# Optimization experiments

Measured on AMD Instinct MI355X. Metric: run time of the kernel, lower is better.

## Reference

```python
import jax, jax.numpy as jnp
import numpy as np

N_NODES = 100000
N_EDGES = 3200000
NUM_GRAPHS = 128
HIDDEN = 32


def setup_inputs() -> dict:
    key = jax.random.key(0)
    ks = jax.random.split(key, 10)
    x1 = jax.random.normal(ks[0], (N_NODES, 1), dtype=jnp.float32)
    x2 = jax.random.normal(ks[1], (N_NODES, 1), dtype=jnp.float32)
    edge_index1 = jax.random.randint(ks[2], (2, N_EDGES), 0, N_NODES, dtype=jnp.int64)
    edge_index2 = jax.random.randint(ks[3], (2, N_EDGES), 0, N_NODES, dtype=jnp.int64)
    batch1 = jnp.sort(jax.random.randint(ks[4], (N_NODES,), 0, NUM_GRAPHS, dtype=jnp.int64))
    batch2 = jnp.sort(jax.random.randint(ks[5], (N_NODES,), 0, NUM_GRAPHS, dtype=jnp.int64))
    W1 = jax.random.normal(ks[6], (1, HIDDEN), dtype=jnp.float32) * 0.5
    b1 = jax.random.normal(ks[7], (HIDDEN,), dtype=jnp.float32) * 0.1
    W2 = jax.random.normal(ks[8], (HIDDEN, HIDDEN), dtype=jnp.float32) * (1.0 / np.sqrt(HIDDEN))
    b2 = jax.random.normal(ks[9], (HIDDEN,), dtype=jnp.float32) * 0.1
    return {"x1": x1, "edge_index1": edge_index1, "batch1": batch1,
            "x2": x2, "edge_index2": edge_index2, "batch2": batch2,
            "W1": W1, "b1": b1, "W2": W2, "b2": b2}


def _gin_conv(x, src, dst, W, b):
    # GINConv with eps=0: nn(x + sum_{j->i} x_j); messages from src aggregated at dst
    agg = jax.ops.segment_sum(x[src], dst, num_segments=N_NODES)
    return jax.nn.relu((x + agg) @ W + b)  # nn = Linear + ReLU


def _encode(x, edge_index, batch, W1, b1, W2, b2):
    src, dst = edge_index[0], edge_index[1]
    h = _gin_conv(x, src, dst, W1, b1)
    # F.relu after conv1 (idempotent after ReLU inside nn, kept for fidelity)
    h = jax.nn.relu(h)
    h = _gin_conv(h, src, dst, W2, b2)
    # global_add_pool: segment-sum nodes by graph id
    return jax.ops.segment_sum(h, batch, num_segments=NUM_GRAPHS)


def reference(x1, edge_index1, batch1, x2, edge_index2, batch2, W1, b1, W2, b2):
    h1 = _encode(x1, edge_index1, batch1, W1, b1, W2, b2)
    h2 = _encode(x2, edge_index2, batch2, W1, b1, W2, b2)
    return jnp.abs(h1 - h2)
```

## Files before the change

### kernel.cpp

```cpp
#include <hip/hip_runtime.h>
#include <hip/hip_bf16.h>
#include <math.h>

#define N_NODES 100000
#define N_EDGES 3200000
#define NUM_GRAPHS 128
#define HIDDEN 32
#define NB 33
#define NPB 128
#define NBKT 782
#define NCHUNK 256
#define EPC (N_EDGES / NCHUNK)
#define SRC_BITS 17
#define SRC_MASK 0x1FFFF
#define S_STRIDE 100096

typedef __attribute__((ext_vector_type(8))) short bf16x8;
typedef __attribute__((ext_vector_type(4))) float f32x4;

__device__ inline unsigned short f2bf(float f) {
    union { float f; unsigned u; } c; c.f = f;
    return (unsigned short)((c.u + 0x7fffu + ((c.u >> 16) & 1u)) >> 16);
}

__global__ void k_setup(const float* __restrict__ W1, const float* __restrict__ b1,
                        float* __restrict__ ts, int* __restrict__ mk,
                        int* __restrict__ cls) {
    __shared__ float t[32];
    __shared__ float tso[32];
    int k = threadIdx.x;
    if (k < 32) {
        float w = W1[k], bb = b1[k];
        int c = (w > 0.f) ? 1 : ((w < 0.f) ? -1 : 0);
        t[k] = (c == 0) ? INFINITY : (-bb / w);
        cls[k] = c;
    }
    __syncthreads();
    if (threadIdx.x == 0) {
        float a[32];
        for (int i = 0; i < 32; ++i) a[i] = t[i];
        for (int i = 1; i < 32; ++i) {
            float key = a[i]; int j = i - 1;
            while (j >= 0 && a[j] > key) { a[j + 1] = a[j]; --j; }
            a[j + 1] = key;
        }
        for (int i = 0; i < 32; ++i) { tso[i] = a[i]; ts[i] = a[i]; }
    }
    __syncthreads();
    if (k < 32) {
        float tk = t[k];
        int m = 0;
        for (int i = 0; i < 32; ++i) m += (tso[i] < tk) ? 1 : 0;
        mk[k] = m;
    }
}

__global__ void k_count2(const int* __restrict__ d1, const int* __restrict__ d2,
                         unsigned* __restrict__ Btot) {
    __shared__ unsigned cnt[NBKT];
    int g = blockIdx.x >> 8, blk = blockIdx.x & 255;
    const int* dst = g ? d2 : d1;
    for (int b = threadIdx.x; b < NBKT; b += blockDim.x) cnt[b] = 0u;
    __syncthreads();
    int e0 = blk * EPC;
    for (int e = e0 + threadIdx.x; e < e0 + EPC; e += blockDim.x)
        atomicAdd(&cnt[((unsigned)dst[e]) >> 7], 1u);
    __syncthreads();
    for (int b = threadIdx.x; b < NBKT; b += blockDim.x)
        if (cnt[b]) atomicAdd(&Btot[g * NBKT + b], cnt[b]);
}

__global__ void k_bscan(const unsigned* __restrict__ Btot,
                        unsigned* __restrict__ Bbase, unsigned* __restrict__ gcur) {
    __shared__ unsigned sc[1024];
    int g = blockIdx.x, t = threadIdx.x;
    unsigned v0 = (t < NBKT) ? Btot[g * NBKT + t] : 0u;
    unsigned v1 = (t + 512 < NBKT) ? Btot[g * NBKT + t + 512] : 0u;
    sc[t] = v0; sc[t + 512] = v1;
    __syncthreads();
    for (int d = 1; d < 1024; d <<= 1) {
        unsigned a0 = (t >= d) ? sc[t - d] : 0u;
        unsigned a1 = (t + 512 >= d) ? sc[t + 512 - d] : 0u;
        __syncthreads();
        sc[t] += a0; sc[t + 512] += a1;
        __syncthreads();
    }
    if (t < NBKT)       { unsigned e = sc[t] - v0;       Bbase[g*NBKT+t]     = e; gcur[g*NBKT+t]     = e; }
    if (t + 512 < NBKT) { unsigned e = sc[t + 512] - v1; Bbase[g*NBKT+t+512] = e; gcur[g*NBKT+t+512] = e; }
}

__global__ void k_scatter2(const int* __restrict__ s1, const int* __restrict__ d1,
                           const int* __restrict__ s2, const int* __restrict__ d2,
                           unsigned* __restrict__ gcur, unsigned* __restrict__ binned) {
    __shared__ unsigned cnt[NBKT];
    __shared__ unsigned pos[NBKT];
    __shared__ unsigned gbase[NBKT];
    __shared__ unsigned sc[1024];
    __shared__ unsigned payload[EPC];
    int g = blockIdx.x >> 8, blk = blockIdx.x & 255;
    const int* src = g ? s2 : s1;
    const int* dst = g ? d2 : d1;
    int t = threadIdx.x;
    for (int b = t; b < NBKT; b += 512) cnt[b] = 0u;
    __syncthreads();
    int e0 = blk * EPC;
    for (int e = e0 + t; e < e0 + EPC; e += 512)
        atomicAdd(&cnt[((unsigned)dst[e]) >> 7], 1u);
    __syncthreads();
    unsigned v0 = (t < NBKT) ? cnt[t] : 0u;
    unsigned v1 = (t + 512 < NBKT) ? cnt[t + 512] : 0u;
    sc[t] = v0; sc[t + 512] = v1;
    __syncthreads();
    for (int d = 1; d < 1024; d <<= 1) {
        unsigned a0 = (t >= d) ? sc[t - d] : 0u;
        unsigned a1 = (t + 512 >= d) ? sc[t + 512 - d] : 0u;
        __syncthreads();
        sc[t] += a0; sc[t + 512] += a1;
        __syncthreads();
    }
    if (t < NBKT) pos[t] = sc[t] - v0;
    if (t + 512 < NBKT) pos[t + 512] = sc[t + 512] - v1;
    __syncthreads();
    for (int b = t; b < NBKT; b += 512) {
        unsigned c = cnt[b];
        gbase[b] = c ? atomicAdd(&gcur[g * NBKT + b], c) : 0u;
        sc[b] = pos[b];
    }
    __syncthreads();
    for (int e = e0 + t; e < e0 + EPC; e += 512) {
        unsigned d = (unsigned)dst[e];
        unsigned p = atomicAdd(&sc[d >> 7], 1u);
        payload[p] = ((d & 127u) << SRC_BITS) | (unsigned)src[e];
    }
    __syncthreads();
    int wave = t >> 6, lane = t & 63;
    size_t gOff = (size_t)g * N_EDGES;
    for (int b = wave; b < NBKT; b += 8) {
        unsigned L = cnt[b], gb = gbase[b], lp = pos[b];
        for (unsigned l = lane; l < L; l += 64)
            binned[gOff + gb + l] = payload[lp + l];
    }
}

__global__ void k_layer1(const float* __restrict__ x1, const float* __restrict__ x2,
                         const unsigned* __restrict__ binned,
                         const unsigned* __restrict__ Bbase, const unsigned* __restrict__ Btot,
                         float* __restrict__ s_all) {
    __shared__ float sloc[NPB];
    int g = blockIdx.x / NBKT, b = blockIdx.x % NBKT;
    const float* x = g ? x2 : x1;
    const unsigned* bn = binned + (size_t)g * N_EDGES;
    float* s = s_all + (size_t)g * S_STRIDE;
    if (threadIdx.x < NPB) sloc[threadIdx.x] = 0.f;
    __syncthreads();
    unsigned beg = Bbase[g * NBKT + b], n = Btot[g * NBKT + b];
    for (unsigned i = threadIdx.x; i < n; i += blockDim.x) {
        unsigned p = bn[beg + i];
        atomicAdd(&sloc[p >> SRC_BITS], x[p & SRC_MASK]);
    }
    __syncthreads();
    if (threadIdx.x < NPB) {
        int node = b * NPB + threadIdx.x;
        if (node < N_NODES) s[node] = sloc[threadIdx.x] + x[node];
    }
}

__global__ void k_layer2(const float* __restrict__ s_all, const unsigned* __restrict__ binned,
                         const unsigned* __restrict__ Bbase, const unsigned* __restrict__ Btot,
                         const int* __restrict__ batch1, const int* __restrict__ batch2,
                         const float* __restrict__ ts, const int* __restrict__ mk,
                         const int* __restrict__ cls,
                         const float* __restrict__ W1, const float* __restrict__ b1,
                         const float* __restrict__ W2, const float* __restrict__ b2,
                         float* __restrict__ pool) {
    __shared__ __align__(16) float hS[NB * NPB];
    __shared__ __align__(16) float hC[NB * NPB];
    __shared__ __align__(16) unsigned short w2t[32 * 40];
    __shared__ float sloc[NPB];
    __shared__ int   batchL[NPB];
    __shared__ float t_sL[32], w1L[32], b1L[32], b2L[32];
    __shared__ int   m1L[32], clsL[32];
    __shared__ float poolacc[4 * 32];
    __shared__ int   slotgid[4];

    const int tid = threadIdx.x;
    const int g = blockIdx.x / NBKT, b = blockIdx.x % NBKT;
    const float* s = s_all + (size_t)g * S_STRIDE;
    const unsigned* bn = binned + (size_t)g * N_EDGES;
    const int* batch = g ? batch2 : batch1;
    float* poolg = pool + (size_t)g * NUM_GRAPHS * HIDDEN;

    for (int i = tid; i < NB * NPB; i += 512) { hS[i] = 0.f; hC[i] = 0.f; }
    if (tid < 32) {
        t_sL[tid] = ts[tid];
        w1L[tid] = W1[tid]; b1L[tid] = b1[tid]; b2L[tid] = b2[tid];
        m1L[tid] = mk[tid] + 1; clsL[tid] = cls[tid];
    }
    if (tid < NPB) {
        int nodeG = b * NPB + tid;
        bool v = nodeG < N_NODES;
        sloc[tid]   = v ? s[nodeG] : 0.f;
        batchL[tid] = v ? batch[nodeG] : -1;
        poolacc[tid] = 0.f;
    }
    if (tid < 4) slotgid[tid] = -1;
    for (int i = tid; i < 1024; i += 512) {
        int j = i & 31, k2 = i >> 5;
        w2t[k2 * 40 + j] = f2bf(W2[j * 32 + k2]);
    }
    __syncthreads();

    unsigned beg = Bbase[g * NBKT + b], n = Btot[g * NBKT + b];
    for (unsigned i = tid; i < n; i += 512) {
        unsigned p = bn[beg + i];
        float sv = s[p & SRC_MASK];
        unsigned dl = p >> SRC_BITS;
        int bk = 0;
        if (t_sL[31] < sv) bk = 32;
        else {
#pragma unroll
            for (int st = 16; st; st >>= 1)
                if (bk + st <= 32 && t_sL[bk + st - 1] < sv) bk += st;
        }
        atomicAdd(&hS[bk * NPB + dl], sv);
        atomicAdd(&hC[bk * NPB + dl], 1.0f);
    }
    __syncthreads();

    if (tid < NPB) {
        int nd = tid; float suf = 0.f;
        for (int j = NB - 1; j >= 0; --j) { suf += hS[j * NPB + nd]; hS[j * NPB + nd] = suf; }
    } else if (tid < 2 * NPB) {
        int nd = tid - NPB; float suf = 0.f;
        for (int j = NB - 1; j >= 0; --j) { suf += hC[j * NPB + nd]; hC[j * NPB + nd] = suf; }
    }
    __syncthreads();

    int nd = tid & 127, kg = tid >> 7;
    bool valid = batchL[nd] >= 0;
    float totS = hS[nd], totC = hC[nd];
    float si = sloc[nd];
    float vf[8];
#pragma unroll
    for (int e = 0; e < 8; ++e) {
        int k = kg * 8 + e;
        int m1 = m1L[k], c = clsL[k];
        float w = w1L[k], bb = b1L[k];
        float SA = (m1 < NB) ? hS[m1 * NPB + nd] : 0.f;
        float CA = (m1 < NB) ? hC[m1 * NPB + nd] : 0.f;
        float agg;
        if (c > 0)      agg = w * SA + bb * CA;
        else if (c < 0) agg = w * (totS - SA) + bb * (totC - CA);
        else            agg = fmaxf(bb, 0.f) * totC;
        vf[e] = valid ? (fmaxf(fmaf(si, w, bb), 0.f) + agg) : 0.f;
    }
    __syncthreads();

    unsigned short* v_lds = (unsigned short*)hC;
    {
        union { bf16x8 v; unsigned short u[8]; } pk;
#pragma unroll
        for (int e = 0; e < 8; ++e) pk.u[e] = f2bf(vf[e]);
        *(bf16x8*)&v_lds[nd * 40 + kg * 8] = pk.v;
    }
    __syncthreads();

    int wv = tid >> 6, lane = tid & 63;
    int kgrp = lane >> 4, col = lane & 15;
    bf16x8 afrag = *(const bf16x8*)&v_lds[(wv * 16 + col) * 40 + kgrp * 8];
    bf16x8 bf0 = *(const bf16x8*)&w2t[col * 40 + kgrp * 8];
    bf16x8 bf1 = *(const bf16x8*)&w2t[(16 + col) * 40 + kgrp * 8];
    f32x4 zero = {0.f, 0.f, 0.f, 0.f};
    f32x4 acc0 = __builtin_amdgcn_mfma_f32_16x16x32_bf16(afrag, bf0, zero, 0, 0, 0);
    f32x4 acc1 = __builtin_amdgcn_mfma_f32_16x16x32_bf16(afrag, bf1, zero, 0, 0, 0);

    int g0 = batchL[wv * 16], g15 = batchL[wv * 16 + 15];
    bool uni = (g0 == g15) && (g0 >= 0);
    if (uni && lane == 0) slotgid[g0 & 3] = g0;
#pragma unroll
    for (int c = 0; c < 2; ++c) {
        f32x4 acc = c ? acc1 : acc0;
        int k2 = c * 16 + col;
        float b2v = b2L[k2];
        float o[4];
#pragma unroll
        for (int r = 0; r < 4; ++r) o[r] = fmaxf(acc[r] + b2v, 0.f);
        if (uni) {
            float s4 = o[0] + o[1] + o[2] + o[3];
            s4 += __shfl_xor(s4, 16, 64);
            s4 += __shfl_xor(s4, 32, 64);
            if (lane < 16) atomicAdd(&poolacc[(g0 & 3) * 32 + k2], s4);
        } else {
#pragma unroll
            for (int r = 0; r < 4; ++r) {
                int nr = wv * 16 + kgrp * 4 + r;
                int gg = batchL[nr];
                if (gg >= 0) {
                    slotgid[gg & 3] = gg;
                    atomicAdd(&poolacc[(gg & 3) * 32 + k2], o[r]);
                }
            }
        }
    }
    __syncthreads();

    if (tid < 128) {
        int slot = tid >> 5, k2 = tid & 31;
        int gg = slotgid[slot];
        if (gg >= 0) atomicAdd(&poolg[gg * HIDDEN + k2], poolacc[slot * 32 + k2]);
    }
}

__global__ void k_absdiff(const float* __restrict__ pool, float* __restrict__ out) {
    int i = blockIdx.x * blockDim.x + threadIdx.x;
    if (i < NUM_GRAPHS * HIDDEN)
        out[i] = fabsf(pool[i] - pool[NUM_GRAPHS * HIDDEN + i]);
}

extern "C" void kernel_launch(void* const* d_in, const int* in_sizes, int n_in,
                              void* d_out, int out_size, void* d_ws, size_t ws_size,
                              hipStream_t stream) {
    const float* x1     = (const float*)d_in[0];
    const int*   ei1    = (const int*)d_in[1];
    const int*   batch1 = (const int*)d_in[2];
    const float* x2     = (const float*)d_in[3];
    const int*   ei2    = (const int*)d_in[4];
    const int*   batch2 = (const int*)d_in[5];
    const float* W1     = (const float*)d_in[6];
    const float* b1     = (const float*)d_in[7];
    const float* W2     = (const float*)d_in[8];
    const float* b2     = (const float*)d_in[9];
    float* out = (float*)d_out;

    const int* src1 = ei1;            const int* dst1 = ei1 + N_EDGES;
    const int* src2 = ei2;            const int* dst2 = ei2 + N_EDGES;

    char* ws = (char*)d_ws;
    size_t off = 0;
    auto alloc = [&](size_t bytes) { char* p = ws + off; off += (bytes + 255) & ~(size_t)255; return p; };
    float*    s_all  = (float*)   alloc((size_t)2 * S_STRIDE * 4);
    unsigned* binned = (unsigned*)alloc((size_t)2 * N_EDGES * 4);
    unsigned* Btot   = (unsigned*)alloc((size_t)2 * NBKT * 4);
    unsigned* Bbase  = (unsigned*)alloc((size_t)2 * NBKT * 4);
    unsigned* gcur   = (unsigned*)alloc((size_t)2 * NBKT * 4);
    float*    pool   = (float*)   alloc((size_t)2 * NUM_GRAPHS * HIDDEN * 4);
    float*    ts     = (float*)   alloc(256);
    int*      mk     = (int*)     alloc(256);
    int*      cls    = (int*)     alloc(256);

    hipMemsetAsync(Btot, 0, (size_t)2 * NBKT * 4, stream);
    hipMemsetAsync(pool, 0, (size_t)2 * NUM_GRAPHS * HIDDEN * 4, stream);
    k_setup<<<1, 64, 0, stream>>>(W1, b1, ts, mk, cls);

    k_count2  <<<2 * NCHUNK, 256, 0, stream>>>(dst1, dst2, Btot);
    k_bscan   <<<2, 512, 0, stream>>>(Btot, Bbase, gcur);
    k_scatter2<<<2 * NCHUNK, 512, 0, stream>>>(src1, dst1, src2, dst2, gcur, binned);
    k_layer1  <<<2 * NBKT, 512, 0, stream>>>(x1, x2, binned, Bbase, Btot, s_all);
    k_layer2  <<<2 * NBKT, 512, 0, stream>>>(s_all, binned, Bbase, Btot, batch1, batch2,
                                             ts, mk, cls, W1, b1, W2, b2, pool);

    k_absdiff<<<(NUM_GRAPHS * HIDDEN + 255) / 256, 256, 0, stream>>>(pool, out);
}
```

Baseline: 365.2 us.

## Replace count-and-scan edge binning with fixed-capacity buckets and batch gathers

```diff
diff --git a/kernel.cpp b/kernel.cpp
--- a/kernel.cpp
+++ b/kernel.cpp
@@ -14,6 +14,8 @@
 #define SRC_BITS 17
 #define SRC_MASK 0x1FFFF
 #define S_STRIDE 100096
+#define CAP 4608
+#define INVALID 0xFFFFFFFFu
 
 typedef __attribute__((ext_vector_type(8))) short bf16x8;
 typedef __attribute__((ext_vector_type(4))) float f32x4;
@@ -53,40 +55,6 @@
         for (int i = 0; i < 32; ++i) m += (tso[i] < tk) ? 1 : 0;
         mk[k] = m;
     }
-}
-
-__global__ void k_count2(const int* __restrict__ d1, const int* __restrict__ d2,
-                         unsigned* __restrict__ Btot) {
-    __shared__ unsigned cnt[NBKT];
-    int g = blockIdx.x >> 8, blk = blockIdx.x & 255;
-    const int* dst = g ? d2 : d1;
-    for (int b = threadIdx.x; b < NBKT; b += blockDim.x) cnt[b] = 0u;
-    __syncthreads();
-    int e0 = blk * EPC;
-    for (int e = e0 + threadIdx.x; e < e0 + EPC; e += blockDim.x)
-        atomicAdd(&cnt[((unsigned)dst[e]) >> 7], 1u);
-    __syncthreads();
-    for (int b = threadIdx.x; b < NBKT; b += blockDim.x)
-        if (cnt[b]) atomicAdd(&Btot[g * NBKT + b], cnt[b]);
-}
-
-__global__ void k_bscan(const unsigned* __restrict__ Btot,
-                        unsigned* __restrict__ Bbase, unsigned* __restrict__ gcur) {
-    __shared__ unsigned sc[1024];
-    int g = blockIdx.x, t = threadIdx.x;
-    unsigned v0 = (t < NBKT) ? Btot[g * NBKT + t] : 0u;
-    unsigned v1 = (t + 512 < NBKT) ? Btot[g * NBKT + t + 512] : 0u;
-    sc[t] = v0; sc[t + 512] = v1;
-    __syncthreads();
-    for (int d = 1; d < 1024; d <<= 1) {
-        unsigned a0 = (t >= d) ? sc[t - d] : 0u;
-        unsigned a1 = (t + 512 >= d) ? sc[t + 512 - d] : 0u;
-        __syncthreads();
-        sc[t] += a0; sc[t + 512] += a1;
-        __syncthreads();
-    }
-    if (t < NBKT)       { unsigned e = sc[t] - v0;       Bbase[g*NBKT+t]     = e; gcur[g*NBKT+t]     = e; }
-    if (t + 512 < NBKT) { unsigned e = sc[t + 512] - v1; Bbase[g*NBKT+t+512] = e; gcur[g*NBKT+t+512] = e; }
 }
 
 __global__ void k_scatter2(const int* __restrict__ s1, const int* __restrict__ d1,
@@ -123,7 +91,7 @@
     __syncthreads();
     for (int b = t; b < NBKT; b += 512) {
         unsigned c = cnt[b];
-        gbase[b] = c ? atomicAdd(&gcur[g * NBKT + b], c) : 0u;
+        gbase[b] = c ? (b * CAP + atomicAdd(&gcur[g * NBKT + b], c)) : 0u;
         sc[b] = pos[b];
     }
     __syncthreads();
@@ -134,39 +102,50 @@
     }
     __syncthreads();
     int wave = t >> 6, lane = t & 63;
-    size_t gOff = (size_t)g * N_EDGES;
+    unsigned* bg = binned + (size_t)g * NBKT * CAP;
     for (int b = wave; b < NBKT; b += 8) {
         unsigned L = cnt[b], gb = gbase[b], lp = pos[b];
         for (unsigned l = lane; l < L; l += 64)
-            binned[gOff + gb + l] = payload[lp + l];
+            bg[gb + l] = payload[lp + l];
     }
 }
 
 __global__ void k_layer1(const float* __restrict__ x1, const float* __restrict__ x2,
                          const unsigned* __restrict__ binned,
-                         const unsigned* __restrict__ Bbase, const unsigned* __restrict__ Btot,
+                         const unsigned* __restrict__ gcur,
                          float* __restrict__ s_all) {
     __shared__ float sloc[NPB];
     int g = blockIdx.x / NBKT, b = blockIdx.x % NBKT;
     const float* x = g ? x2 : x1;
-    const unsigned* bn = binned + (size_t)g * N_EDGES;
+    const unsigned* bp = binned + (size_t)g * NBKT * CAP + (size_t)b * CAP;
     float* s = s_all + (size_t)g * S_STRIDE;
-    if (threadIdx.x < NPB) sloc[threadIdx.x] = 0.f;
-    __syncthreads();
-    unsigned beg = Bbase[g * NBKT + b], n = Btot[g * NBKT + b];
-    for (unsigned i = threadIdx.x; i < n; i += blockDim.x) {
-        unsigned p = bn[beg + i];
-        atomicAdd(&sloc[p >> SRC_BITS], x[p & SRC_MASK]);
-    }
-    __syncthreads();
-    if (threadIdx.x < NPB) {
-        int node = b * NPB + threadIdx.x;
-        if (node < N_NODES) s[node] = sloc[threadIdx.x] + x[node];
+    int tid = threadIdx.x;
+    if (tid < NPB) sloc[tid] = 0.f;
+    __syncthreads();
+    unsigned n = gcur[g * NBKT + b];
+    for (unsigned base = 0; base < n; base += 4096) {
+        unsigned p[8]; float xv[8];
+#pragma unroll
+        for (int e = 0; e < 8; ++e) {
+            unsigned i = base + e * 512 + tid;
+            p[e] = (i < n) ? bp[i] : INVALID;
+        }
+#pragma unroll
+        for (int e = 0; e < 8; ++e)
+            xv[e] = (p[e] != INVALID) ? x[p[e] & SRC_MASK] : 0.f;
+#pragma unroll
+        for (int e = 0; e < 8; ++e)
+            if (p[e] != INVALID) atomicAdd(&sloc[p[e] >> SRC_BITS], xv[e]);
+    }
+    __syncthreads();
+    if (tid < NPB) {
+        int node = b * NPB + tid;
+        if (node < N_NODES) s[node] = sloc[tid] + x[node];
     }
 }
 
 __global__ void k_layer2(const float* __restrict__ s_all, const unsigned* __restrict__ binned,
-                         const unsigned* __restrict__ Bbase, const unsigned* __restrict__ Btot,
+                         const unsigned* __restrict__ gcur,
                          const int* __restrict__ batch1, const int* __restrict__ batch2,
                          const float* __restrict__ ts, const int* __restrict__ mk,
                          const int* __restrict__ cls,
@@ -186,7 +165,7 @@
     const int tid = threadIdx.x;
     const int g = blockIdx.x / NBKT, b = blockIdx.x % NBKT;
     const float* s = s_all + (size_t)g * S_STRIDE;
-    const unsigned* bn = binned + (size_t)g * N_EDGES;
+    const unsigned* bp = binned + (size_t)g * NBKT * CAP + (size_t)b * CAP;
     const int* batch = g ? batch2 : batch1;
     float* poolg = pool + (size_t)g * NUM_GRAPHS * HIDDEN;
 
@@ -210,20 +189,32 @@
     }
     __syncthreads();
 
-    unsigned beg = Bbase[g * NBKT + b], n = Btot[g * NBKT + b];
-    for (unsigned i = tid; i < n; i += 512) {
-        unsigned p = bn[beg + i];
-        float sv = s[p & SRC_MASK];
-        unsigned dl = p >> SRC_BITS;
-        int bk = 0;
-        if (t_sL[31] < sv) bk = 32;
-        else {
-#pragma unroll
-            for (int st = 16; st; st >>= 1)
-                if (bk + st <= 32 && t_sL[bk + st - 1] < sv) bk += st;
-        }
-        atomicAdd(&hS[bk * NPB + dl], sv);
-        atomicAdd(&hC[bk * NPB + dl], 1.0f);
+    unsigned n = gcur[g * NBKT + b];
+    for (unsigned base = 0; base < n; base += 4096) {
+        unsigned p[8]; float sv[8];
+#pragma unroll
+        for (int e = 0; e < 8; ++e) {
+            unsigned i = base + e * 512 + tid;
+            p[e] = (i < n) ? bp[i] : INVALID;
+        }
+#pragma unroll
+        for (int e = 0; e < 8; ++e)
+            sv[e] = (p[e] != INVALID) ? s[p[e] & SRC_MASK] : 0.f;
+#pragma unroll
+        for (int e = 0; e < 8; ++e) {
+            if (p[e] == INVALID) continue;
+            float v = sv[e];
+            unsigned dl = p[e] >> SRC_BITS;
+            int bk = 0;
+            if (t_sL[31] < v) bk = 32;
+            else {
+#pragma unroll
+                for (int st = 16; st; st >>= 1)
+                    if (bk + st <= 32 && t_sL[bk + st - 1] < v) bk += st;
+            }
+            atomicAdd(&hS[bk * NPB + dl], v);
+            atomicAdd(&hC[bk * NPB + dl], 1.0f);
+        }
     }
     __syncthreads();
 
@@ -339,24 +330,20 @@
     size_t off = 0;
     auto alloc = [&](size_t bytes) { char* p = ws + off; off += (bytes + 255) & ~(size_t)255; return p; };
     float*    s_all  = (float*)   alloc((size_t)2 * S_STRIDE * 4);
-    unsigned* binned = (unsigned*)alloc((size_t)2 * N_EDGES * 4);
-    unsigned* Btot   = (unsigned*)alloc((size_t)2 * NBKT * 4);
-    unsigned* Bbase  = (unsigned*)alloc((size_t)2 * NBKT * 4);
+    unsigned* binned = (unsigned*)alloc((size_t)2 * NBKT * CAP * 4);
     unsigned* gcur   = (unsigned*)alloc((size_t)2 * NBKT * 4);
     float*    pool   = (float*)   alloc((size_t)2 * NUM_GRAPHS * HIDDEN * 4);
     float*    ts     = (float*)   alloc(256);
     int*      mk     = (int*)     alloc(256);
     int*      cls    = (int*)     alloc(256);
 
-    hipMemsetAsync(Btot, 0, (size_t)2 * NBKT * 4, stream);
+    hipMemsetAsync(gcur, 0, (size_t)2 * NBKT * 4, stream);
     hipMemsetAsync(pool, 0, (size_t)2 * NUM_GRAPHS * HIDDEN * 4, stream);
     k_setup<<<1, 64, 0, stream>>>(W1, b1, ts, mk, cls);
 
-    k_count2  <<<2 * NCHUNK, 256, 0, stream>>>(dst1, dst2, Btot);
-    k_bscan   <<<2, 512, 0, stream>>>(Btot, Bbase, gcur);
     k_scatter2<<<2 * NCHUNK, 512, 0, stream>>>(src1, dst1, src2, dst2, gcur, binned);
-    k_layer1  <<<2 * NBKT, 512, 0, stream>>>(x1, x2, binned, Bbase, Btot, s_all);
-    k_layer2  <<<2 * NBKT, 512, 0, stream>>>(s_all, binned, Bbase, Btot, batch1, batch2,
+    k_layer1  <<<2 * NBKT, 512, 0, stream>>>(x1, x2, binned, gcur, s_all);
+    k_layer2  <<<2 * NBKT, 512, 0, stream>>>(s_all, binned, gcur, batch1, batch2,
                                              ts, mk, cls, W1, b1, W2, b2, pool);
 
     k_absdiff<<<(NUM_GRAPHS * HIDDEN + 255) / 256, 256, 0, stream>>>(pool, out);
```

Result: faster. 350.9 us (-3.9%).
